# Performance work log

Measured on AMD Instinct MI355X. Metric: run time of the kernel, lower is better.

## Reference

```python
import jax, jax.numpy as jnp
import numpy as np

TOTAL = 16777216  # total jagged values
SEGS = 8192       # number of segments (prefix_sum length)


def setup_inputs() -> dict:
    key = jax.random.key(0)
    k1, k2 = jax.random.split(key)
    logits = jax.random.normal(k1, (TOTAL,), dtype=jnp.float32)
    prefix_sum = jnp.sort(jax.random.randint(k2, (SEGS,), 0, TOTAL, dtype=jnp.int32))
    # prefix_sum holds cumulative (exclusive) segment end offsets; last must equal TOTAL
    prefix_sum = prefix_sum.at[-1].set(TOTAL)
    return {"logits": logits, "prefix_sum": prefix_sum}


def reference(logits, prefix_sum):
    n = logits.shape[0]
    num_segs = prefix_sum.shape[0]
    # element i belongs to segment j where prefix_sum[j-1] <= i < prefix_sum[j]
    seg = jnp.searchsorted(prefix_sum, jnp.arange(n, dtype=prefix_sum.dtype), side="right")
    # numerically stable per-segment log-softmax
    seg_max = jax.ops.segment_max(logits, seg, num_segments=num_segs)
    shifted = logits - seg_max[seg]
    seg_sumexp = jax.ops.segment_sum(jnp.exp(shifted), seg, num_segments=num_segs)
    return shifted - jnp.log(seg_sumexp)[seg]
```

## Files before the change

### kernel.cpp

```cpp
#include <hip/hip_runtime.h>
#include <math.h>

#define TPB 256

__device__ __forceinline__ float max4(float4 v) {
    return fmaxf(fmaxf(v.x, v.y), fmaxf(v.z, v.w));
}

__device__ __forceinline__ void combine(float& m, float& l, float mo, float lo) {
    float mn = fmaxf(m, mo);
    float a = (l  > 0.0f) ? l  * __expf(m  - mn) : 0.0f;
    float b = (lo > 0.0f) ? lo * __expf(mo - mn) : 0.0f;
    m = mn;
    l = a + b;
}

__global__ __launch_bounds__(TPB) void jls_kernel(
    const float* __restrict__ x,
    const int* __restrict__ prefix,
    float* __restrict__ out)
{
    const int seg   = blockIdx.x;
    const int start = (seg == 0) ? 0 : prefix[seg - 1];
    const int end   = prefix[seg];
    if (end <= start) return;

    const int tid = threadIdx.x;

    int a0 = (start + 3) & ~3;  if (a0 > end) a0 = end;
    int a1 = end & ~3;          if (a1 < a0) a1 = a0;
    const float4* __restrict__ x4 = (const float4*)x;
    const int v0 = a0 >> 2, v1 = a1 >> 2;

    float m0 = -INFINITY, l0 = 0.0f;
    float m1 = -INFINITY, l1 = 0.0f;
    int i = v0 + tid;
    for (; i + TPB < v1; i += 2 * TPB) {
        float4 a = x4[i];
        float4 b = x4[i + TPB];
        float am = max4(a), bm = max4(b);
        if (am > m0) { l0 *= __expf(m0 - am); m0 = am; }
        l0 += __expf(a.x - m0) + __expf(a.y - m0) + __expf(a.z - m0) + __expf(a.w - m0);
        if (bm > m1) { l1 *= __expf(m1 - bm); m1 = bm; }
        l1 += __expf(b.x - m1) + __expf(b.y - m1) + __expf(b.z - m1) + __expf(b.w - m1);
    }
    if (i < v1) {
        float4 a = x4[i];
        float am = max4(a);
        if (am > m0) { l0 *= __expf(m0 - am); m0 = am; }
        l0 += __expf(a.x - m0) + __expf(a.y - m0) + __expf(a.z - m0) + __expf(a.w - m0);
    }
    for (int j = start + tid; j < a0; j += TPB) {
        float v = x[j];
        if (v > m0) { l0 *= __expf(m0 - v); m0 = v; }
        l0 += __expf(v - m0);
    }
    for (int j = a1 + tid; j < end; j += TPB) {
        float v = x[j];
        if (v > m1) { l1 *= __expf(m1 - v); m1 = v; }
        l1 += __expf(v - m1);
    }
    combine(m0, l0, m1, l1);

    #pragma unroll
    for (int off = 32; off > 0; off >>= 1) {
        float mo = __shfl_xor(m0, off, 64);
        float lo = __shfl_xor(l0, off, 64);
        combine(m0, l0, mo, lo);
    }
    __shared__ float sm[4], sl[4];
    if ((tid & 63) == 0) { sm[tid >> 6] = m0; sl[tid >> 6] = l0; }
    __syncthreads();
    float M = sm[0], L = sl[0];
    combine(M, L, sm[1], sl[1]);
    combine(M, L, sm[2], sl[2]);
    combine(M, L, sm[3], sl[3]);

    const float c = M + __logf(L);

    float4* __restrict__ o4 = (float4*)out;
    i = v0 + tid;
    for (; i + TPB < v1; i += 2 * TPB) {
        float4 a = x4[i];
        float4 b = x4[i + TPB];
        float4 ra, rb;
        ra.x = a.x - c; ra.y = a.y - c; ra.z = a.z - c; ra.w = a.w - c;
        rb.x = b.x - c; rb.y = b.y - c; rb.z = b.z - c; rb.w = b.w - c;
        o4[i] = ra;
        o4[i + TPB] = rb;
    }
    if (i < v1) {
        float4 a = x4[i];
        float4 ra;
        ra.x = a.x - c; ra.y = a.y - c; ra.z = a.z - c; ra.w = a.w - c;
        o4[i] = ra;
    }
    for (int j = start + tid; j < a0; j += TPB) out[j] = x[j] - c;
    for (int j = a1 + tid;   j < end; j += TPB) out[j] = x[j] - c;
}

extern "C" void kernel_launch(void* const* d_in, const int* in_sizes, int n_in,
                              void* d_out, int out_size, void* d_ws, size_t ws_size,
                              hipStream_t stream) {
    const float* logits = (const float*)d_in[0];
    const int*   prefix = (const int*)d_in[1];
    float*       out    = (float*)d_out;
    const int num_segs  = in_sizes[1];

    jls_kernel<<<num_segs, TPB, 0, stream>>>(logits, prefix, out);
}
```

Before: 120.0 us.

## Cache first segment chunk in registers and use nontemporal output stores

```diff
diff --git a/kernel.cpp b/kernel.cpp
--- a/kernel.cpp
+++ b/kernel.cpp
@@ -2,9 +2,17 @@
 #include <math.h>
 
 #define TPB 256
+#define NC  8
+
+typedef float vfloat4 __attribute__((ext_vector_type(4)));
 
 __device__ __forceinline__ float max4(float4 v) {
     return fmaxf(fmaxf(v.x, v.y), fmaxf(v.z, v.w));
+}
+
+__device__ __forceinline__ void nt_store4(float4 r, float4* p) {
+    vfloat4 v = {r.x, r.y, r.z, r.w};
+    __builtin_nontemporal_store(v, (vfloat4*)p);
 }
 
 __device__ __forceinline__ void combine(float& m, float& l, float mo, float lo) {
@@ -13,6 +21,12 @@
     float b = (lo > 0.0f) ? lo * __expf(mo - mn) : 0.0f;
     m = mn;
     l = a + b;
+}
+
+__device__ __forceinline__ void acc4(float4 a, float& m, float& l) {
+    float am = max4(a);
+    if (am > m) { l *= __expf(m - am); m = am; }
+    l += __expf(a.x - m) + __expf(a.y - m) + __expf(a.z - m) + __expf(a.w - m);
 }
 
 __global__ __launch_bounds__(TPB) void jls_kernel(
@@ -32,24 +46,35 @@
     const float4* __restrict__ x4 = (const float4*)x;
     const int v0 = a0 >> 2, v1 = a1 >> 2;
 
+    const int i0 = v0 + tid;
+
+    float4 rc[NC];
+    bool   hv[NC];
+    #pragma unroll
+    for (int k = 0; k < NC; ++k) {
+        hv[k] = (i0 + k * TPB) < v1;
+        if (hv[k]) rc[k] = x4[i0 + k * TPB];
+    }
+
     float m0 = -INFINITY, l0 = 0.0f;
     float m1 = -INFINITY, l1 = 0.0f;
-    int i = v0 + tid;
+    #pragma unroll
+    for (int k = 0; k < NC; ++k) {
+        if (hv[k]) {
+            if (k & 1) acc4(rc[k], m1, l1);
+            else       acc4(rc[k], m0, l0);
+        }
+    }
+
+    int i = i0 + NC * TPB;
     for (; i + TPB < v1; i += 2 * TPB) {
         float4 a = x4[i];
         float4 b = x4[i + TPB];
-        float am = max4(a), bm = max4(b);
-        if (am > m0) { l0 *= __expf(m0 - am); m0 = am; }
-        l0 += __expf(a.x - m0) + __expf(a.y - m0) + __expf(a.z - m0) + __expf(a.w - m0);
-        if (bm > m1) { l1 *= __expf(m1 - bm); m1 = bm; }
-        l1 += __expf(b.x - m1) + __expf(b.y - m1) + __expf(b.z - m1) + __expf(b.w - m1);
+        acc4(a, m0, l0);
+        acc4(b, m1, l1);
     }
-    if (i < v1) {
-        float4 a = x4[i];
-        float am = max4(a);
-        if (am > m0) { l0 *= __expf(m0 - am); m0 = am; }
-        l0 += __expf(a.x - m0) + __expf(a.y - m0) + __expf(a.z - m0) + __expf(a.w - m0);
-    }
+    if (i < v1) acc4(x4[i], m0, l0);
+
     for (int j = start + tid; j < a0; j += TPB) {
         float v = x[j];
         if (v > m0) { l0 *= __expf(m0 - v); m0 = v; }
@@ -79,24 +104,33 @@
     const float c = M + __logf(L);
 
     float4* __restrict__ o4 = (float4*)out;
-    i = v0 + tid;
+    #pragma unroll
+    for (int k = 0; k < NC; ++k) {
+        if (hv[k]) {
+            float4 r;
+            r.x = rc[k].x - c; r.y = rc[k].y - c; r.z = rc[k].z - c; r.w = rc[k].w - c;
+            nt_store4(r, &o4[i0 + k * TPB]);
+        }
+    }
+
+    i = i0 + NC * TPB;
     for (; i + TPB < v1; i += 2 * TPB) {
         float4 a = x4[i];
         float4 b = x4[i + TPB];
         float4 ra, rb;
         ra.x = a.x - c; ra.y = a.y - c; ra.z = a.z - c; ra.w = a.w - c;
         rb.x = b.x - c; rb.y = b.y - c; rb.z = b.z - c; rb.w = b.w - c;
-        o4[i] = ra;
-        o4[i + TPB] = rb;
+        nt_store4(ra, &o4[i]);
+        nt_store4(rb, &o4[i + TPB]);
     }
     if (i < v1) {
         float4 a = x4[i];
         float4 ra;
         ra.x = a.x - c; ra.y = a.y - c; ra.z = a.z - c; ra.w = a.w - c;
-        o4[i] = ra;
+        nt_store4(ra, &o4[i]);
     }
-    for (int j = start + tid; j < a0; j += TPB) out[j] = x[j] - c;
-    for (int j = a1 + tid;   j < end; j += TPB) out[j] = x[j] - c;
+    for (int j = start + tid; j < a0; j += TPB) __builtin_nontemporal_store(x[j] - c, &out[j]);
+    for (int j = a1 + tid;   j < end; j += TPB) __builtin_nontemporal_store(x[j] - c, &out[j]);
 }
 
 extern "C" void kernel_launch(void* const* d_in, const int* in_sizes, int n_in,
```

Result: faster. 114.8 us (-4.3%).
